# Kernel optimization log

Measured on AMD Instinct MI355X. Metric: run time of the kernel, lower is better.

The kernel has to match this reference:

```python
import jax, jax.numpy as jnp
import numpy as np

EPS = 0.001  # additive floor applied after relu, as in the torch code


def setup_inputs() -> dict:
    key = jax.random.key(0)
    kA, kB, kW = jax.random.split(key, 3)
    M, N, C, H, W = 512, 64, 128, 8, 8
    A = jax.random.normal(kA, (M, C, H, W), dtype=jnp.float32)
    B = jax.random.normal(kB, (N, C, H, W), dtype=jnp.float32)
    Wg = jax.random.normal(kW, (C, C), dtype=jnp.float32) * 0.01  # Wg.data.normal_(0.0, 0.01)
    return {"A": A, "B": B, "Wg": Wg}


def reference(A, B, Wg):
    # Faithful vectorization of MIMOcom.get_source_dst_max(A, B, dir=True).
    # Torch loops i,j over HxW: B0 = B[:, i, j, :]; G = B0 @ Wg;
    # combination[m, n, p] = sum_c A[m, p, c] * G[n, c]; running max over (i, j).
    M, C, H, W = A.shape
    N = B.shape[0]
    P = H * W
    Af = jnp.transpose(A, (0, 2, 3, 1)).reshape(M, P, C)  # [M, P, C]
    Bf = jnp.transpose(B, (0, 2, 3, 1)).reshape(N, P, C)  # [N, Q, C]
    G = Bf @ Wg                                           # [N, Q, D]
    scores = jnp.einsum('mpd,nqd->mnpq', Af, G)           # [M, N, P, Q]
    comb_max = scores.max(axis=-1)                        # max over B positions q
    return jax.nn.relu(comb_max) + EPS                    # [M, N, P]
```

## Files before the change

kernel.cpp:

```cpp
#include <hip/hip_runtime.h>
#include <hip/hip_bf16.h>
#include <stdint.h>

typedef __attribute__((ext_vector_type(8))) short bf16x8;
typedef __attribute__((ext_vector_type(16))) float f32x16;
using bf16 = __hip_bfloat16;

static constexpr int Mdim = 512;
static constexpr int Ndim = 64;
static constexpr int Cdim = 128;
static constexpr int Pdim = 64;
static constexpr float EPS_ADD = 0.001f;

#define SB0 __builtin_amdgcn_sched_barrier(0)

__device__ __forceinline__ void gll16(const void* gsrc, void* ldst) {
    const __attribute__((address_space(1))) unsigned int* g =
        (const __attribute__((address_space(1))) unsigned int*)gsrc;
    __attribute__((address_space(3))) unsigned int* l =
        (__attribute__((address_space(3))) unsigned int*)(uintptr_t)ldst;
    __builtin_amdgcn_global_load_lds(g, l, 16, 0, 0);
}

__global__ void prep_kernel(const float* __restrict__ A, const float* __restrict__ B,
                            const float* __restrict__ Wg,
                            bf16* __restrict__ Afrag, bf16* __restrict__ Gfrag) {
    __shared__ float lds[128 * 65];
    const int t = threadIdx.x;

    if (blockIdx.x < 512) {
        const int m = blockIdx.x;
        const float* __restrict__ Am = A + (size_t)m * (Cdim * Pdim);
#pragma unroll
        for (int i = 0; i < 8; ++i) {
            int v = t + i * 256;
            int gidx = v * 4;
            int c = gidx >> 6, p = gidx & 63;
            float4 val = *reinterpret_cast<const float4*>(Am + gidx);
            float* dst = &lds[c * 65 + p];
            dst[0] = val.x; dst[1] = val.y; dst[2] = val.z; dst[3] = val.w;
        }
        __syncthreads();

        unsigned* __restrict__ dst32 = (unsigned*)(Afrag + (size_t)m * 8192);
#pragma unroll
        for (int i = 0; i < 16; ++i) {
            int pr = t + i * 256;
            int p = pr >> 6;
            int c = (pr & 63) << 1;
            float f0 = lds[c * 65 + p];
            float f1 = lds[(c + 1) * 65 + p];
            union { bf16 hh[2]; unsigned u; } pk;
            pk.hh[0] = __float2bfloat16(f0);
            pk.hh[1] = __float2bfloat16(f1);
            int h = p >> 5, l31 = p & 31;
            int ks = c >> 4, hi = (c >> 3) & 1, e = c & 7;
            dst32[h * 2048 + ks * 256 + hi * 128 + l31 * 4 + (e >> 1)] = pk.u;
        }
    } else {
        const int nb = blockIdx.x - 512;
        const int n  = nb >> 2;
        const int q0 = (nb & 3) * 16;
        const float* __restrict__ Bn = B + (size_t)n * (Cdim * Pdim);
#pragma unroll
        for (int i = 0; i < 8; ++i) {
            int v = t + i * 256;
            int gidx = v * 4;
            int c = gidx >> 6, q = gidx & 63;
            float4 val = *reinterpret_cast<const float4*>(Bn + gidx);
            float* dst = &lds[c * 65 + q];
            dst[0] = val.x; dst[1] = val.y; dst[2] = val.z; dst[3] = val.w;
        }
        __syncthreads();

        const int d  = t & 127;
        const int qb = q0 + (t >> 7) * 8;
        float acc[8] = {0.f, 0.f, 0.f, 0.f, 0.f, 0.f, 0.f, 0.f};
        for (int c = 0; c < 128; ++c) {
            float w = Wg[c * 128 + d];
#pragma unroll
            for (int qi = 0; qi < 8; ++qi)
                acc[qi] = fmaf(lds[c * 65 + qb + qi], w, acc[qi]);
        }
        bf16* __restrict__ gdst = Gfrag + (size_t)n * 8192;
        const int ks = d >> 4, hi = (d >> 3) & 1, e = d & 7;
#pragma unroll
        for (int qi = 0; qi < 8; ++qi) {
            int q = qb + qi;
            int qt = q >> 5, l31 = q & 31;
            gdst[qt * 4096 + ks * 512 + hi * 256 + l31 * 8 + e] = __float2bfloat16(acc[qi]);
        }
    }
}

__global__ __launch_bounds__(256, 2)
void gemm_max_kernel(const bf16* __restrict__ Afrag, const bf16* __restrict__ Gfrag,
                     float* __restrict__ out) {
    __shared__ bf16 sG[3][8192];
    const int tid  = threadIdx.x;
    const int lane = tid & 63;
    const int wv   = tid >> 6;
    const int mi = wv >> 1, h = wv & 1;
    const int l31 = lane & 31, hi = lane >> 5;
    const int mg = blockIdx.x & 127;
    const int bn = blockIdx.x >> 7;
    const int m0 = mg * 4 + mi * 2;

    bf16x8 a[2][8];
#pragma unroll
    for (int u = 0; u < 2; ++u) {
        const bf16* Ap = Afrag + (size_t)(m0 + u) * 8192 + h * 4096 + lane * 8;
#pragma unroll
        for (int ks = 0; ks < 8; ++ks)
            a[u][ks] = *reinterpret_cast<const bf16x8*>(Ap + ks * 512);
    }
    asm volatile("" ::: "memory");

    const char* Gsrc = (const char*)(Gfrag + (size_t)(bn * 16) * 8192);
    auto stageG = [&](int s) {
        char* dst = (char*)&sG[s % 3][0];
        const char* src = Gsrc + (size_t)s * 16384;
#pragma unroll
        for (int i = 0; i < 4; ++i) {
            int f = (i * 256 + tid) * 16;
            gll16(src + f, dst + f);
        }
    };
    stageG(0);
    stageG(1);

    const f32x16 z16 = {0.f,0.f,0.f,0.f,0.f,0.f,0.f,0.f,0.f,0.f,0.f,0.f,0.f,0.f,0.f,0.f};
    f32x16 acc0, acc1;
    bf16x8 gfA[8], gfB[8];

    auto ldgf = [&](bf16x8 (&g)[8], const char* base) {
#pragma unroll
        for (int ks = 0; ks < 8; ++ks)
            g[ks] = *reinterpret_cast<const bf16x8*>(base + ks * 1024);
    };
    auto mmcl = [&](const bf16x8 (&gf)[8]) {
        __builtin_amdgcn_s_setprio(1);
        acc0 = __builtin_amdgcn_mfma_f32_32x32x16_bf16(gf[0], a[0][0], z16, 0, 0, 0);
        acc1 = __builtin_amdgcn_mfma_f32_32x32x16_bf16(gf[0], a[1][0], z16, 0, 0, 0);
#pragma unroll
        for (int ks = 1; ks < 8; ++ks) {
            acc0 = __builtin_amdgcn_mfma_f32_32x32x16_bf16(gf[ks], a[0][ks], acc0, 0, 0, 0);
            acc1 = __builtin_amdgcn_mfma_f32_32x32x16_bf16(gf[ks], a[1][ks], acc1, 0, 0, 0);
        }
        __builtin_amdgcn_s_setprio(0);
    };
    auto red16 = [&](const f32x16& v) -> float {
        float x0 = fmaxf(v[0], v[1]),  x1 = fmaxf(v[2], v[3]);
        float x2 = fmaxf(v[4], v[5]),  x3 = fmaxf(v[6], v[7]);
        float x4 = fmaxf(v[8], v[9]),  x5 = fmaxf(v[10], v[11]);
        float x6 = fmaxf(v[12], v[13]), x7 = fmaxf(v[14], v[15]);
        x0 = fmaxf(x0, x1); x2 = fmaxf(x2, x3);
        x4 = fmaxf(x4, x5); x6 = fmaxf(x6, x7);
        return fmaxf(fmaxf(x0, x2), fmaxf(x4, x6));
    };

#define BODY(S, WV, DOSTAGE, DOPREF)                                          \
    __builtin_amdgcn_s_barrier(); SB0;                                        \
    if (DOSTAGE) stageG((S) + 2);                                             \
    ldgf(gfB, (const char*)&sG[(S) % 3][0] + 8192 + lane * 16);               \
    mmcl(gfA);                                                                \
    asm volatile("s_waitcnt vmcnt(" #WV ")" ::: "memory"); SB0;               \
    if (DOPREF) ldgf(gfA, (const char*)&sG[((S) + 1) % 3][0] + lane * 16);    \
    {                                                                         \
        float t0 = red16(acc0), t1 = red16(acc1);                             \
        mmcl(gfB);                                                            \
        t0 = fmaxf(t0, red16(acc0)); t1 = fmaxf(t1, red16(acc1));             \
        t0 = fmaxf(t0, __shfl_xor(t0, 32));                                   \
        t1 = fmaxf(t1, __shfl_xor(t1, 32));                                   \
        const int n = bn * 16 + (S);                                          \
        const float sv = hi ? t1 : t0;                                        \
        out[(size_t)(m0 + hi) * 4096 + n * 64 + h * 32 + l31] =               \
            fmaxf(sv, 0.f) + EPS_ADD;                                         \
    }

    asm volatile("s_waitcnt vmcnt(4)" ::: "memory");
    __builtin_amdgcn_s_barrier(); SB0;
    ldgf(gfA, (const char*)&sG[0][0] + lane * 16);

    BODY(0, 4, 1, 1)
    BODY(1, 5, 1, 1)
    BODY(2, 5, 1, 1)
    BODY(3, 5, 1, 1)
    BODY(4, 5, 1, 1)
    BODY(5, 5, 1, 1)
    BODY(6, 5, 1, 1)
    BODY(7, 5, 1, 1)
    BODY(8, 5, 1, 1)
    BODY(9, 5, 1, 1)
    BODY(10, 5, 1, 1)
    BODY(11, 5, 1, 1)
    BODY(12, 5, 1, 1)
    BODY(13, 5, 1, 1)
    BODY(14, 1, 0, 1)
    BODY(15, 2, 0, 0)
#undef BODY
}

extern "C" void kernel_launch(void* const* d_in, const int* in_sizes, int n_in,
                              void* d_out, int out_size, void* d_ws, size_t ws_size,
                              hipStream_t stream) {
    const float* A  = (const float*)d_in[0];
    const float* B  = (const float*)d_in[1];
    const float* Wg = (const float*)d_in[2];
    float* out = (float*)d_out;

    bf16* Afrag = (bf16*)d_ws;
    bf16* Gfrag = (bf16*)((char*)d_ws + (size_t)Mdim * Pdim * Cdim * sizeof(bf16));

    prep_kernel<<<768, 256, 0, stream>>>(A, B, Wg, Afrag, Gfrag);
    gemm_max_kernel<<<512, 256, 0, stream>>>(Afrag, Gfrag, out);
}
```

Before: 47.48 us.

## Split N across twice as many blocks and use double-buffered G staging

The GEMM-max grid doubles from 512 to 1024 blocks, so each block covers 8 N values instead of 16. Launch bounds now target 3 blocks per SIMD. The triple-buffered LDS pipeline with register prefetch of G fragments becomes a two-buffer scheme that loads both G halves at the start of each step. The aim is more concurrent work and less LDS per block to hide latency. The cost is loading each A fragment into registers twice as often. There is also a possible write-after-read race, because the next stage is issued before the barrier that guards the buffer other waves may still be reading.

Result: slower. 51.61 us (+8.7%).

```diff
diff --git a/kernel.cpp b/kernel.cpp
--- a/kernel.cpp
+++ b/kernel.cpp
@@ -93,10 +93,10 @@
     }
 }
 
-__global__ __launch_bounds__(256, 2)
+__global__ __launch_bounds__(256, 3)
 void gemm_max_kernel(const bf16* __restrict__ Afrag, const bf16* __restrict__ Gfrag,
                      float* __restrict__ out) {
-    __shared__ bf16 sG[3][8192];
+    __shared__ bf16 sG[2][8192];
     const int tid  = threadIdx.x;
     const int lane = tid & 63;
     const int wv   = tid >> 6;
@@ -116,9 +116,9 @@
     }
     asm volatile("" ::: "memory");
 
-    const char* Gsrc = (const char*)(Gfrag + (size_t)(bn * 16) * 8192);
+    const char* Gsrc = (const char*)(Gfrag + (size_t)(bn * 8) * 8192);
     auto stageG = [&](int s) {
-        char* dst = (char*)&sG[s % 3][0];
+        char* dst = (char*)&sG[s & 1][0];
         const char* src = Gsrc + (size_t)s * 16384;
 #pragma unroll
         for (int i = 0; i < 4; ++i) {
@@ -126,12 +126,10 @@
             gll16(src + f, dst + f);
         }
     };
-    stageG(0);
-    stageG(1);
 
     const f32x16 z16 = {0.f,0.f,0.f,0.f,0.f,0.f,0.f,0.f,0.f,0.f,0.f,0.f,0.f,0.f,0.f,0.f};
     f32x16 acc0, acc1;
-    bf16x8 gfA[8], gfB[8];
+    bf16x8 gf0[8], gf1[8];
 
     auto ldgf = [&](bf16x8 (&g)[8], const char* base) {
 #pragma unroll
@@ -159,45 +157,37 @@
         return fmaxf(fmaxf(x0, x2), fmaxf(x4, x6));
     };
 
-#define BODY(S, WV, DOSTAGE, DOPREF)                                          \
+#define BODY(S, WV, DOSTAGE)                                                  \
+    if (DOSTAGE) stageG((S) + 1);                                             \
+    asm volatile("s_waitcnt vmcnt(" #WV ")" ::: "memory");                    \
     __builtin_amdgcn_s_barrier(); SB0;                                        \
-    if (DOSTAGE) stageG((S) + 2);                                             \
-    ldgf(gfB, (const char*)&sG[(S) % 3][0] + 8192 + lane * 16);               \
-    mmcl(gfA);                                                                \
-    asm volatile("s_waitcnt vmcnt(" #WV ")" ::: "memory"); SB0;               \
-    if (DOPREF) ldgf(gfA, (const char*)&sG[((S) + 1) % 3][0] + lane * 16);    \
+    ldgf(gf0, (const char*)&sG[(S) & 1][0] + lane * 16);                      \
+    ldgf(gf1, (const char*)&sG[(S) & 1][0] + 8192 + lane * 16);               \
+    mmcl(gf0);                                                                \
     {                                                                         \
         float t0 = red16(acc0), t1 = red16(acc1);                             \
-        mmcl(gfB);                                                            \
+        mmcl(gf1);                                                            \
         t0 = fmaxf(t0, red16(acc0)); t1 = fmaxf(t1, red16(acc1));             \
         t0 = fmaxf(t0, __shfl_xor(t0, 32));                                   \
         t1 = fmaxf(t1, __shfl_xor(t1, 32));                                   \
-        const int n = bn * 16 + (S);                                          \
+        const int n = bn * 8 + (S);                                           \
         const float sv = hi ? t1 : t0;                                        \
         out[(size_t)(m0 + hi) * 4096 + n * 64 + h * 32 + l31] =               \
             fmaxf(sv, 0.f) + EPS_ADD;                                         \
     }
 
-    asm volatile("s_waitcnt vmcnt(4)" ::: "memory");
+    stageG(0);
+    asm volatile("s_waitcnt vmcnt(0)" ::: "memory");
     __builtin_amdgcn_s_barrier(); SB0;
-    ldgf(gfA, (const char*)&sG[0][0] + lane * 16);
-
-    BODY(0, 4, 1, 1)
-    BODY(1, 5, 1, 1)
-    BODY(2, 5, 1, 1)
-    BODY(3, 5, 1, 1)
-    BODY(4, 5, 1, 1)
-    BODY(5, 5, 1, 1)
-    BODY(6, 5, 1, 1)
-    BODY(7, 5, 1, 1)
-    BODY(8, 5, 1, 1)
-    BODY(9, 5, 1, 1)
-    BODY(10, 5, 1, 1)
-    BODY(11, 5, 1, 1)
-    BODY(12, 5, 1, 1)
-    BODY(13, 5, 1, 1)
-    BODY(14, 1, 0, 1)
-    BODY(15, 2, 0, 0)
+
+    BODY(0, 4, 1)
+    BODY(1, 5, 1)
+    BODY(2, 5, 1)
+    BODY(3, 5, 1)
+    BODY(4, 5, 1)
+    BODY(5, 5, 1)
+    BODY(6, 5, 1)
+    BODY(7, 1, 0)
 #undef BODY
 }
 
@@ -213,5 +203,5 @@
     bf16* Gfrag = (bf16*)((char*)d_ws + (size_t)Mdim * Pdim * Cdim * sizeof(bf16));
 
     prep_kernel<<<768, 256, 0, stream>>>(A, B, Wg, Afrag, Gfrag);
-    gemm_max_kernel<<<512, 256, 0, stream>>>(Afrag, Gfrag, out);
-}
+    gemm_max_kernel<<<1024, 256, 0, stream>>>(Afrag, Gfrag, out);
+}
```
